# Kernel tuning notes

Measured on AMD Instinct MI355X. Metric: run time of the kernel, lower is better.

Reference implementation:

```python
import jax, jax.numpy as jnp
import numpy as np

EMBED_DIM = 1024
NUM_HEADS = 16
HEAD_DIM = EMBED_DIM // NUM_HEADS
ROPE_BASE = 10000.0


def _rope_cos_sin(seq_len, dim, dtype=jnp.float32):
    inv_freq = 1.0 / (ROPE_BASE ** (jnp.arange(0, dim, 2, dtype=jnp.float32) / dim))
    pos = jnp.arange(seq_len, dtype=jnp.float32)
    freqs = jnp.outer(pos, inv_freq)              # [S, dim/2]
    emb = jnp.concatenate([freqs, freqs], axis=-1)  # [S, dim]
    return jnp.cos(emb).astype(dtype), jnp.sin(emb).astype(dtype)


def _rotate_half(x):
    half = x.shape[-1] // 2
    return jnp.concatenate([-x[..., half:], x[..., :half]], axis=-1)


def setup_inputs() -> dict:
    key = jax.random.key(0)
    ks = jax.random.split(key, 12)
    B, S, E = 4, 2048, EMBED_DIM
    std = 1.0 / np.sqrt(E)
    inp = {
        'query': jax.random.normal(ks[0], (B, S, E), jnp.float32),
        'key': jax.random.normal(ks[1], (B, S, E), jnp.float32),
        'value': jax.random.normal(ks[2], (B, S, E), jnp.float32),
        'Wq': jax.random.uniform(ks[3], (E, E), jnp.float32, -std, std),
        'bq': jax.random.uniform(ks[4], (E,), jnp.float32, -std, std),
        'Wk': jax.random.uniform(ks[5], (E, E), jnp.float32, -std, std),
        'bk': jax.random.uniform(ks[6], (E,), jnp.float32, -std, std),
        'Wv': jax.random.uniform(ks[7], (E, E), jnp.float32, -std, std),
        'bv': jax.random.uniform(ks[8], (E,), jnp.float32, -std, std),
        'Wo': jax.random.uniform(ks[9], (E, E), jnp.float32, -std, std),
        'bo': jax.random.uniform(ks[10], (E,), jnp.float32, -std, std),
    }
    return inp


def reference(query, key, value, Wq, bq, Wk, bk, Wv, bv, Wo, bo):
    B, Sq, E = query.shape
    Sk = key.shape[1]
    H, D = NUM_HEADS, HEAD_DIM
    scale = D ** -0.5

    q = query @ Wq.T + bq
    k = key @ Wk.T + bk
    v = value @ Wv.T + bv

    # [B, H, S, D]
    q = q.reshape(B, Sq, H, D).transpose(0, 2, 1, 3)
    k = k.reshape(B, Sk, H, D).transpose(0, 2, 1, 3)
    v = v.reshape(B, Sk, H, D).transpose(0, 2, 1, 3)

    cos, sin = _rope_cos_sin(Sq, D, q.dtype)  # [S, D]; module slices by seq_len_q for both
    cos = cos[None, None]  # [1,1,S,D]
    sin = sin[None, None]
    q = q * cos + _rotate_half(q) * sin
    k = k * cos + _rotate_half(k) * sin

    scores = jnp.einsum('bhqd,bhkd->bhqk', q, k) * scale
    attn = jax.nn.softmax(scores, axis=-1)  # dropout p=0.0 -> identity
    out = jnp.einsum('bhqk,bhkd->bhqd', attn, v)
    out = out.transpose(0, 2, 1, 3).reshape(B, Sq, E)
    out = out @ Wo.T + bo
    attn_avg = attn.mean(axis=1)  # [B, Sq, Sk]
    return out, attn_avg
```

## Files before the change

### kernel.cpp

```cpp
#include <hip/hip_runtime.h>
#include <math.h>

#define TB 4
#define TS 2048
#define TE 1024
#define TH 16
#define TD 64
#define TM_ (TB*TS)

#define WS_Q   0
#define WS_K   8388608
#define WS_L   16777216
#define WS_TAB 16908288

typedef __attribute__((ext_vector_type(8))) short bf16x8;
typedef __attribute__((ext_vector_type(4))) float f32x4;

static __device__ inline unsigned fbits(float x) {
    union { float f; unsigned u; } v; v.f = x; return v.u;
}
static __device__ inline float bits2f(unsigned u) {
    union { unsigned u; float f; } v; v.u = u; return v.f;
}
static __device__ inline unsigned pack_rhu(float a, float b) {
    return __builtin_amdgcn_perm(fbits(b) + 0x8000u, fbits(a) + 0x8000u, 0x07060302u);
}
static __device__ inline short bf16s(float x) {
    return (short)((fbits(x) + 0x8000u) >> 16);
}
static __device__ inline void split2(float x0, float x1, unsigned& hp, unsigned& lp) {
    unsigned u0 = fbits(x0) + 0x8000u, u1 = fbits(x1) + 0x8000u;
    hp = __builtin_amdgcn_perm(u1, u0, 0x07060302u);
    float h0 = bits2f(u0 & 0xffff0000u);
    float h1 = bits2f(u1 & 0xffff0000u);
    lp = pack_rhu(x0 - h0, x1 - h1);
}

template<int MODE>
__global__ __launch_bounds__(256, 2)
void gemm_nt(const float* __restrict__ X, const float* __restrict__ W,
             const float* __restrict__ bias, float* __restrict__ out)
{
    __shared__ short Ah[128][40], Al[128][40];
    __shared__ short Bh[128][40], Bl[128][40];

    const int tid  = threadIdx.x;
    const int lane = tid & 63;
    const int wv   = tid >> 6;
    const int t16  = lane & 15;
    const int quad = lane >> 4;
    const int wm   = (wv >> 1) * 64;
    const int wn   = (wv & 1) * 64;
    const int m0 = blockIdx.y * 128;
    const int n0 = blockIdx.x * 128;
    const int K = TE, N = TE;

    const int srow = tid >> 1;
    const int skc  = (tid & 1) * 16;
    const float* Xp = X + (size_t)(m0 + srow) * K + skc;
    const float* Wp = W + (size_t)(n0 + srow) * K + skc;

    f32x4 acc[4][4];
    #pragma unroll
    for (int i = 0; i < 4; ++i)
        #pragma unroll
        for (int j = 0; j < 4; ++j) acc[i][j] = (f32x4){0.f, 0.f, 0.f, 0.f};

    for (int kt = 0; kt < K; kt += 32) {
        __syncthreads();
        {
            const float* xp = Xp + kt;
            float4 x0 = *(const float4*)(xp);
            float4 x1 = *(const float4*)(xp + 4);
            float4 x2 = *(const float4*)(xp + 8);
            float4 x3 = *(const float4*)(xp + 12);
            const float* wp = Wp + kt;
            float4 w0 = *(const float4*)(wp);
            float4 w1 = *(const float4*)(wp + 4);
            float4 w2 = *(const float4*)(wp + 8);
            float4 w3 = *(const float4*)(wp + 12);

            unsigned H[8], L[8];
            split2(x0.x, x0.y, H[0], L[0]);
            split2(x0.z, x0.w, H[1], L[1]);
            split2(x1.x, x1.y, H[2], L[2]);
            split2(x1.z, x1.w, H[3], L[3]);
            split2(x2.x, x2.y, H[4], L[4]);
            split2(x2.z, x2.w, H[5], L[5]);
            split2(x3.x, x3.y, H[6], L[6]);
            split2(x3.z, x3.w, H[7], L[7]);
            *(uint4*)&Ah[srow][skc]     = make_uint4(H[0], H[1], H[2], H[3]);
            *(uint4*)&Ah[srow][skc + 8] = make_uint4(H[4], H[5], H[6], H[7]);
            *(uint4*)&Al[srow][skc]     = make_uint4(L[0], L[1], L[2], L[3]);
            *(uint4*)&Al[srow][skc + 8] = make_uint4(L[4], L[5], L[6], L[7]);

            split2(w0.x, w0.y, H[0], L[0]);
            split2(w0.z, w0.w, H[1], L[1]);
            split2(w1.x, w1.y, H[2], L[2]);
            split2(w1.z, w1.w, H[3], L[3]);
            split2(w2.x, w2.y, H[4], L[4]);
            split2(w2.z, w2.w, H[5], L[5]);
            split2(w3.x, w3.y, H[6], L[6]);
            split2(w3.z, w3.w, H[7], L[7]);
            *(uint4*)&Bh[srow][skc]     = make_uint4(H[0], H[1], H[2], H[3]);
            *(uint4*)&Bh[srow][skc + 8] = make_uint4(H[4], H[5], H[6], H[7]);
            *(uint4*)&Bl[srow][skc]     = make_uint4(L[0], L[1], L[2], L[3]);
            *(uint4*)&Bl[srow][skc + 8] = make_uint4(L[4], L[5], L[6], L[7]);
        }
        __syncthreads();

        bf16x8 ah[4], al[4], bh[4], bl[4];
        #pragma unroll
        for (int i = 0; i < 4; ++i) {
            ah[i] = *(const bf16x8*)&Ah[wm + i * 16 + t16][quad * 8];
            al[i] = *(const bf16x8*)&Al[wm + i * 16 + t16][quad * 8];
            bh[i] = *(const bf16x8*)&Bh[wn + i * 16 + t16][quad * 8];
            bl[i] = *(const bf16x8*)&Bl[wn + i * 16 + t16][quad * 8];
        }
        #pragma unroll
        for (int i = 0; i < 4; ++i)
            #pragma unroll
            for (int j = 0; j < 4; ++j) {
                acc[i][j] = __builtin_amdgcn_mfma_f32_16x16x32_bf16(ah[i], bh[j], acc[i][j], 0, 0, 0);
                acc[i][j] = __builtin_amdgcn_mfma_f32_16x16x32_bf16(al[i], bh[j], acc[i][j], 0, 0, 0);
                acc[i][j] = __builtin_amdgcn_mfma_f32_16x16x32_bf16(ah[i], bl[j], acc[i][j], 0, 0, 0);
            }
    }

    if (MODE == 2) {
        short* o16 = (short*)out;
        const int b = m0 >> 11;
        const int sbase0 = (m0 & 2047) + wm + quad * 4;
        #pragma unroll
        for (int j = 0; j < 4; ++j) {
            const int n = n0 + wn + j * 16 + t16;
            const int h = n >> 6, d = n & 63;
            const float bv = bias[n];
            const size_t base = ((size_t)(b * TH + h) * TD + d) * TS;
            #pragma unroll
            for (int i = 0; i < 4; ++i) {
                const int s = sbase0 + i * 16;
                uint2 p = make_uint2(pack_rhu(acc[i][j][0] + bv, acc[i][j][1] + bv),
                                     pack_rhu(acc[i][j][2] + bv, acc[i][j][3] + bv));
                *(uint2*)(o16 + base + s) = p;
            }
        }
        return;
    }

    #pragma unroll
    for (int j = 0; j < 4; ++j) {
        const int n = n0 + wn + j * 16 + t16;
        const float bv = bias[n];
        if (MODE == 0) {
            #pragma unroll
            for (int i = 0; i < 4; ++i)
                #pragma unroll
                for (int r = 0; r < 4; ++r) {
                    const int m = m0 + wm + i * 16 + quad * 4 + r;
                    out[(size_t)m * N + n] = acc[i][j][r] + bv;
                }
        } else {
            const int h = n >> 6, d = n & 63;
            #pragma unroll
            for (int i = 0; i < 4; ++i)
                #pragma unroll
                for (int r = 0; r < 4; ++r) {
                    const int m = m0 + wm + i * 16 + quad * 4 + r;
                    const int bb_ = m >> 11, s = m & 2047;
                    out[((size_t)(bb_ * TH + h) * TS + s) * TD + d] = acc[i][j][r] + bv;
                }
        }
    }
}

__global__ void rope_table(float* __restrict__ tab)
{
    const int idx = blockIdx.x * 256 + threadIdx.x;
    const int d = idx & 31, s = idx >> 5;
    const float e = (float)(2 * d) / 64.0f;
    const float inv = 1.0f / powf(10000.0f, e);
    const float a = (float)s * inv;
    tab[2 * idx + 0] = cosf(a);
    tab[2 * idx + 1] = sinf(a);
}

__global__ void rope_apply(float* __restrict__ Q, float* __restrict__ Kv,
                           const float* __restrict__ tab)
{
    const int idx = blockIdx.x * 256 + threadIdx.x;
    const int half = TB * TH * TS * 32;
    float* P = (idx < half) ? Q : Kv;
    const int u = idx & (half - 1);
    const int d = u & 31;
    const int s = (u >> 5) & 2047;
    const int bh = u >> 16;
    const size_t base = (size_t)bh * (TS * TD) + (size_t)s * TD;
    const float c  = tab[2 * (s * 32 + d) + 0];
    const float sn = tab[2 * (s * 32 + d) + 1];
    const float x0 = P[base + d], x1 = P[base + d + 32];
    P[base + d]      = x0 * c - x1 * sn;
    P[base + d + 32] = x1 * c + x0 * sn;
}

__global__ __launch_bounds__(512, 4)
void attn_flash(const float* __restrict__ Q, const float* __restrict__ Kg,
                const short* __restrict__ VT, float* __restrict__ O,
                float* __restrict__ Ls)
{
    __shared__ short KhL[4096], KlL[4096];
    __shared__ short VtL[4096];
    __shared__ short PsL[8192];

    const int tid  = threadIdx.x;
    const int lane = tid & 63;
    const int wv   = tid >> 6;
    const int t16  = lane & 15;
    const int quad = lane >> 4;
    const int q0w  = wv * 16;

    const int L   = blockIdx.x + 16 * blockIdx.y + 256 * blockIdx.z;
    const int xcd = L & 7;
    const int i_  = L >> 3;
    const int qt  = i_ & 15;
    const int g   = (xcd << 3) | (i_ >> 4);
    const int h   = g & 15;
    const int b   = g >> 4;

    const int q0 = qt * 128;
    const int bh = b * TH + h;
    const size_t hoff = (size_t)bh * TS * TD;
    const float* Kr = Kg + hoff;
    const short* Vth = VT + (size_t)bh * TD * TS;

    const int cx0 = ((quad) ^ (t16 & 7)) * 8;
    const int cx1 = ((4 + quad) ^ (t16 & 7)) * 8;

    const float qsc = 0.125f * 1.44269504f;
    bf16x8 qfh[2], qfl[2];
    {
        const float* qp = Q + hoff + (size_t)(q0 + q0w + t16) * TD;
        #pragma unroll
        for (int ks = 0; ks < 2; ++ks) {
            float4 a = *(const float4*)(qp + ks * 32 + quad * 8);
            float4 c = *(const float4*)(qp + ks * 32 + quad * 8 + 4);
            union { unsigned u[4]; bf16x8 v; } H, Lo;
            split2(a.x * qsc, a.y * qsc, H.u[0], Lo.u[0]);
            split2(a.z * qsc, a.w * qsc, H.u[1], Lo.u[1]);
            split2(c.x * qsc, c.y * qsc, H.u[2], Lo.u[2]);
            split2(c.z * qsc, c.w * qsc, H.u[3], Lo.u[3]);
            qfh[ks] = H.v; qfl[ks] = Lo.v;
        }
    }

    float lsum[4] = {0.f, 0.f, 0.f, 0.f};
    f32x4 o_acc[4];
    #pragma unroll
    for (int dt = 0; dt < 4; ++dt) o_acc[dt] = (f32x4){0.f, 0.f, 0.f, 0.f};

    const int krow = tid >> 3;
    const int kch  = tid & 7;
    const int ksl  = (kch ^ (krow & 7)) * 8;

    for (int j0 = 0; j0 < TS; j0 += 64) {
        __syncthreads();
        {
            const float* kp = Kr + (size_t)(j0 + krow) * TD + kch * 8;
            float4 a = *(const float4*)kp;
            float4 c = *(const float4*)(kp + 4);
            unsigned H[4], Lo[4];
            split2(a.x, a.y, H[0], Lo[0]);
            split2(a.z, a.w, H[1], Lo[1]);
            split2(c.x, c.y, H[2], Lo[2]);
            split2(c.z, c.w, H[3], Lo[3]);
            *(uint4*)&KhL[krow * 64 + ksl] = make_uint4(H[0], H[1], H[2], H[3]);
            *(uint4*)&KlL[krow * 64 + ksl] = make_uint4(Lo[0], Lo[1], Lo[2], Lo[3]);
            uint4 vv = *(const uint4*)(Vth + (size_t)krow * TS + j0 + kch * 8);
            *(uint4*)&VtL[krow * 64 + ksl] = vv;
        }
        __syncthreads();

        f32x4 sc[4];
        #pragma unroll
        for (int t = 0; t < 4; ++t) sc[t] = (f32x4){0.f, 0.f, 0.f, 0.f};
        #pragma unroll
        for (int t = 0; t < 4; ++t) {
            const int rb = (t * 16 + t16) * 64;
            bf16x8 kh0 = *(const bf16x8*)&KhL[rb + cx0];
            bf16x8 kl0 = *(const bf16x8*)&KlL[rb + cx0];
            sc[t] = __builtin_amdgcn_mfma_f32_16x16x32_bf16(qfh[0], kh0, sc[t], 0, 0, 0);
            sc[t] = __builtin_amdgcn_mfma_f32_16x16x32_bf16(qfh[0], kl0, sc[t], 0, 0, 0);
            sc[t] = __builtin_amdgcn_mfma_f32_16x16x32_bf16(qfl[0], kh0, sc[t], 0, 0, 0);
            bf16x8 kh1 = *(const bf16x8*)&KhL[rb + cx1];
            bf16x8 kl1 = *(const bf16x8*)&KlL[rb + cx1];
            sc[t] = __builtin_amdgcn_mfma_f32_16x16x32_bf16(qfh[1], kh1, sc[t], 0, 0, 0);
            sc[t] = __builtin_amdgcn_mfma_f32_16x16x32_bf16(qfh[1], kl1, sc[t], 0, 0, 0);
            sc[t] = __builtin_amdgcn_mfma_f32_16x16x32_bf16(qfl[1], kh1, sc[t], 0, 0, 0);
        }

        #pragma unroll
        for (int t = 0; t < 4; ++t) {
            float p0 = __builtin_amdgcn_exp2f(sc[t][0]);
            float p1 = __builtin_amdgcn_exp2f(sc[t][1]);
            float p2 = __builtin_amdgcn_exp2f(sc[t][2]);
            float p3 = __builtin_amdgcn_exp2f(sc[t][3]);
            lsum[0] += p0; lsum[1] += p1; lsum[2] += p2; lsum[3] += p3;
            const int cb = 2 * t + (t16 >> 3);
            const int co = t16 & 7;
            const int r0 = q0w + quad * 4;
            PsL[(r0 + 0) * 64 + ((cb ^ ((r0 + 0) & 7)) * 8) + co] = bf16s(p0);
            PsL[(r0 + 1) * 64 + ((cb ^ ((r0 + 1) & 7)) * 8) + co] = bf16s(p1);
            PsL[(r0 + 2) * 64 + ((cb ^ ((r0 + 2) & 7)) * 8) + co] = bf16s(p2);
            PsL[(r0 + 3) * 64 + ((cb ^ ((r0 + 3) & 7)) * 8) + co] = bf16s(p3);
        }

        {
            const int pr = (q0w + t16) * 64;
            bf16x8 pa0 = *(const bf16x8*)&PsL[pr + cx0];
            #pragma unroll
            for (int dt = 0; dt < 4; ++dt) {
                bf16x8 vb = *(const bf16x8*)&VtL[(dt * 16 + t16) * 64 + cx0];
                o_acc[dt] = __builtin_amdgcn_mfma_f32_16x16x32_bf16(pa0, vb, o_acc[dt], 0, 0, 0);
            }
            bf16x8 pa1 = *(const bf16x8*)&PsL[pr + cx1];
            #pragma unroll
            for (int dt = 0; dt < 4; ++dt) {
                bf16x8 vb = *(const bf16x8*)&VtL[(dt * 16 + t16) * 64 + cx1];
                o_acc[dt] = __builtin_amdgcn_mfma_f32_16x16x32_bf16(pa1, vb, o_acc[dt], 0, 0, 0);
            }
        }
    }

    #pragma unroll
    for (int r = 0; r < 4; ++r) {
        #pragma unroll
        for (int off = 1; off < 16; off <<= 1)
            lsum[r] += __shfl_xor(lsum[r], off, 16);
    }

    #pragma unroll
    for (int r = 0; r < 4; ++r) {
        const int row = q0 + q0w + quad * 4 + r;
        const float inv = 1.0f / lsum[r];
        #pragma unroll
        for (int dt = 0; dt < 4; ++dt)
            O[((size_t)(b * TS) + row) * TE + h * TD + dt * 16 + t16] = o_acc[dt][r] * inv;
        if (t16 == 0)
            Ls[(size_t)bh * TS + row] = lsum[r];
    }
}

__global__ __launch_bounds__(256, 2)
void attn_avg_k(const float* __restrict__ Q, const float* __restrict__ Kg,
                const float* __restrict__ Ls, float* __restrict__ AV)
{
    __shared__ short Qt[128][72];
    __shared__ short Kt[128][72];
    __shared__ float ML[TH][128];

    const int tid  = threadIdx.x;
    const int lane = tid & 63;
    const int wv   = tid >> 6;
    const int t16  = lane & 15;
    const int quad = lane >> 4;
    const int wq = (wv >> 1) * 64;
    const int wj = (wv & 1) * 64;

    const int j0 = blockIdx.x * 128;
    const int q0 = blockIdx.y * 128;
    const int b  = blockIdx.z;

    #pragma unroll
    for (int i = 0; i < 8; ++i) {
        const int u = tid + 256 * i;
        const int h = u >> 7, r = u & 127;
        ML[h][r] = 1.0f / Ls[(size_t)(b * TH + h) * TS + q0 + r];
    }

    f32x4 acc[4][4];
    #pragma unroll
    for (int mt = 0; mt < 4; ++mt)
        #pragma unroll
        for (int nt = 0; nt < 4; ++nt) acc[mt][nt] = (f32x4){0.f, 0.f, 0.f, 0.f};

    const float qscale = 0.125f * 1.44269504f;

    for (int h = 0; h < TH; ++h) {
        __syncthreads();
        const size_t hoff = (size_t)(b * TH + h) * TS * TD;
        #pragma unroll
        for (int i = 0; i < 8; ++i) {
            const int f = tid + 256 * i;
            const int row = f >> 4;
            const int dq = (f & 15) * 4;
            float4 qv = *(const float4*)(Q + hoff + (size_t)(q0 + row) * TD + dq);
            uint2 qp = make_uint2(pack_rhu(qv.x * qscale, qv.y * qscale),
                                  pack_rhu(qv.z * qscale, qv.w * qscale));
            *(uint2*)&Qt[row][dq] = qp;
            float4 kv = *(const float4*)(Kg + hoff + (size_t)(j0 + row) * TD + dq);
            uint2 kp = make_uint2(pack_rhu(kv.x, kv.y), pack_rhu(kv.z, kv.w));
            *(uint2*)&Kt[row][dq] = kp;
        }
        __syncthreads();

        f32x4 sc[4][4];
        #pragma unroll
        for (int mt = 0; mt < 4; ++mt)
            #pragma unroll
            for (int nt = 0; nt < 4; ++nt) sc[mt][nt] = (f32x4){0.f, 0.f, 0.f, 0.f};
        #pragma unroll
        for (int ks = 0; ks < 2; ++ks) {
            bf16x8 af[4], bf[4];
            #pragma unroll
            for (int mt = 0; mt < 4; ++mt)
                af[mt] = *(const bf16x8*)&Qt[wq + mt * 16 + t16][ks * 32 + quad * 8];
            #pragma unroll
            for (int nt = 0; nt < 4; ++nt)
                bf[nt] = *(const bf16x8*)&Kt[wj + nt * 16 + t16][ks * 32 + quad * 8];
            #pragma unroll
            for (int mt = 0; mt < 4; ++mt)
                #pragma unroll
                for (int nt = 0; nt < 4; ++nt)
                    sc[mt][nt] = __builtin_amdgcn_mfma_f32_16x16x32_bf16(af[mt], bf[nt], sc[mt][nt], 0, 0, 0);
        }

        #pragma unroll
        for (int mt = 0; mt < 4; ++mt) {
            const int rl = wq + mt * 16 + quad * 4;
            const float lv[4] = {ML[h][rl], ML[h][rl + 1], ML[h][rl + 2], ML[h][rl + 3]};
            #pragma unroll
            for (int nt = 0; nt < 4; ++nt)
                #pragma unroll
                for (int r = 0; r < 4; ++r)
                    acc[mt][nt][r] = fmaf(__builtin_amdgcn_exp2f(sc[mt][nt][r]), lv[r], acc[mt][nt][r]);
        }
    }

    const float inv_h = 1.0f / (float)TH;
    #pragma unroll
    for (int mt = 0; mt < 4; ++mt) {
        #pragma unroll
        for (int r = 0; r < 4; ++r) {
            const int row = q0 + wq + mt * 16 + quad * 4 + r;
            #pragma unroll
            for (int nt = 0; nt < 4; ++nt) {
                const int col = j0 + wj + nt * 16 + t16;
                AV[((size_t)b * TS + row) * TS + col] = acc[mt][nt][r] * inv_h;
            }
        }
    }
}

extern "C" void kernel_launch(void* const* d_in, const int* in_sizes, int n_in,
                              void* d_out, int out_size, void* d_ws, size_t ws_size,
                              hipStream_t stream)
{
    const float* query = (const float*)d_in[0];
    const float* key   = (const float*)d_in[1];
    const float* value = (const float*)d_in[2];
    const float* Wq = (const float*)d_in[3];
    const float* bq = (const float*)d_in[4];
    const float* Wk = (const float*)d_in[5];
    const float* bk = (const float*)d_in[6];
    const float* Wv = (const float*)d_in[7];
    const float* bv = (const float*)d_in[8];
    const float* Wo = (const float*)d_in[9];
    const float* bo = (const float*)d_in[10];

    float* ws  = (float*)d_ws;
    float* Qr  = ws + WS_Q;
    float* Kr  = ws + WS_K;
    float* Lsf = ws + WS_L;
    float* tab = ws + WS_TAB;

    float* out  = (float*)d_out;
    float* attn = out + (size_t)TB * TS * TE;
    short* VT = (short*)attn;
    float* Ow = attn + 4194304;

    dim3 blk(256);
    dim3 gproj(TE / 128, TM_ / 128);

    gemm_nt<1><<<gproj, blk, 0, stream>>>(query, Wq, bq, Qr);
    gemm_nt<1><<<gproj, blk, 0, stream>>>(key,   Wk, bk, Kr);
    gemm_nt<2><<<gproj, blk, 0, stream>>>(value, Wv, bv, (float*)VT);
    rope_table<<<dim3(256), blk, 0, stream>>>(tab);
    rope_apply<<<dim3(32768), blk, 0, stream>>>(Qr, Kr, tab);
    attn_flash<<<dim3(TS / 128, TH, TB), dim3(512), 0, stream>>>(Qr, Kr, VT, Ow, Lsf);
    gemm_nt<0><<<gproj, blk, 0, stream>>>(Ow, Wo, bo, out);
    attn_avg_k<<<dim3(TS / 128, TS / 128, TB), blk, 0, stream>>>(Qr, Kr, Lsf, attn);
}
```

Baseline: 677.3 us.

## Pre-split weights and RoPE outputs into bf16 hi/lo once, prefetch K/V tiles

Adds a kernel that converts all four weight matrices into packed bf16 hi/lo pairs once, so the projection GEMMs load ready-made bf16 B tiles instead of re-splitting fp32 weights in every block. RoPE now also applies the softmax scale to Q, splits Q/K into swizzled bf16 hi/lo rows in place, and the attention and attn-average kernels read these directly. The flash kernel additionally register-prefetches the next K/V tile. This removes repeated conversion work and halves the global bytes read for K/Q, at the cost of an extra pass and scratch space carved from the output buffer.

Measured after the change: 685.7 us. Within noise of the previous version (+1.2%).

```diff
diff --git a/kernel.cpp b/kernel.cpp
--- a/kernel.cpp
+++ b/kernel.cpp
@@ -36,9 +36,35 @@
     lp = pack_rhu(x0 - h0, x1 - h1);
 }
 
+__global__ __launch_bounds__(256, 4)
+void wsplit(const float* __restrict__ W0, const float* __restrict__ W1,
+            const float* __restrict__ W2, const float* __restrict__ W3,
+            short* __restrict__ dst)
+{
+    const int idx = blockIdx.x * 256 + threadIdx.x;
+    const int t = idx & 31;
+    const int n = (idx >> 5) & 1023;
+    const int w = idx >> 15;
+    const float* W = (w == 0) ? W0 : (w == 1) ? W1 : (w == 2) ? W2 : W3;
+    const float* sp = W + (size_t)n * 1024 + t * 32;
+    short* dp = dst + ((size_t)(w * 1024 + n)) * 2048 + t * 64;
+    #pragma unroll
+    for (int c = 0; c < 4; ++c) {
+        float4 a = *(const float4*)(sp + c * 8);
+        float4 b = *(const float4*)(sp + c * 8 + 4);
+        unsigned H[4], L[4];
+        split2(a.x, a.y, H[0], L[0]);
+        split2(a.z, a.w, H[1], L[1]);
+        split2(b.x, b.y, H[2], L[2]);
+        split2(b.z, b.w, H[3], L[3]);
+        *(uint4*)(dp + c * 8)      = make_uint4(H[0], H[1], H[2], H[3]);
+        *(uint4*)(dp + 32 + c * 8) = make_uint4(L[0], L[1], L[2], L[3]);
+    }
+}
+
 template<int MODE>
 __global__ __launch_bounds__(256, 2)
-void gemm_nt(const float* __restrict__ X, const float* __restrict__ W,
+void gemm_nt(const float* __restrict__ X, const short* __restrict__ Wsp,
              const float* __restrict__ bias, float* __restrict__ out)
 {
     __shared__ short Ah[128][40], Al[128][40];
@@ -58,7 +84,7 @@
     const int srow = tid >> 1;
     const int skc  = (tid & 1) * 16;
     const float* Xp = X + (size_t)(m0 + srow) * K + skc;
-    const float* Wp = W + (size_t)(n0 + srow) * K + skc;
+    const short* Wp = Wsp + (size_t)(n0 + srow) * 2048 + skc;
 
     f32x4 acc[4][4];
     #pragma unroll
@@ -74,11 +100,11 @@
             float4 x1 = *(const float4*)(xp + 4);
             float4 x2 = *(const float4*)(xp + 8);
             float4 x3 = *(const float4*)(xp + 12);
-            const float* wp = Wp + kt;
-            float4 w0 = *(const float4*)(wp);
-            float4 w1 = *(const float4*)(wp + 4);
-            float4 w2 = *(const float4*)(wp + 8);
-            float4 w3 = *(const float4*)(wp + 12);
+            const short* wp = Wp + kt * 2;
+            uint4 wh0 = *(const uint4*)(wp);
+            uint4 wh1 = *(const uint4*)(wp + 8);
+            uint4 wl0 = *(const uint4*)(wp + 32);
+            uint4 wl1 = *(const uint4*)(wp + 40);
 
             unsigned H[8], L[8];
             split2(x0.x, x0.y, H[0], L[0]);
@@ -94,18 +120,10 @@
             *(uint4*)&Al[srow][skc]     = make_uint4(L[0], L[1], L[2], L[3]);
             *(uint4*)&Al[srow][skc + 8] = make_uint4(L[4], L[5], L[6], L[7]);
 
-            split2(w0.x, w0.y, H[0], L[0]);
-            split2(w0.z, w0.w, H[1], L[1]);
-            split2(w1.x, w1.y, H[2], L[2]);
-            split2(w1.z, w1.w, H[3], L[3]);
-            split2(w2.x, w2.y, H[4], L[4]);
-            split2(w2.z, w2.w, H[5], L[5]);
-            split2(w3.x, w3.y, H[6], L[6]);
-            split2(w3.z, w3.w, H[7], L[7]);
-            *(uint4*)&Bh[srow][skc]     = make_uint4(H[0], H[1], H[2], H[3]);
-            *(uint4*)&Bh[srow][skc + 8] = make_uint4(H[4], H[5], H[6], H[7]);
-            *(uint4*)&Bl[srow][skc]     = make_uint4(L[0], L[1], L[2], L[3]);
-            *(uint4*)&Bl[srow][skc + 8] = make_uint4(L[4], L[5], L[6], L[7]);
+            *(uint4*)&Bh[srow][skc]     = wh0;
+            *(uint4*)&Bh[srow][skc + 8] = wh1;
+            *(uint4*)&Bl[srow][skc]     = wl0;
+            *(uint4*)&Bl[srow][skc + 8] = wl1;
         }
         __syncthreads();
 
@@ -185,26 +203,48 @@
     tab[2 * idx + 1] = sinf(a);
 }
 
-__global__ void rope_apply(float* __restrict__ Q, float* __restrict__ Kv,
-                           const float* __restrict__ tab)
+__global__ __launch_bounds__(256, 2)
+void rope_split(float* __restrict__ Q, float* __restrict__ Kv,
+                const float* __restrict__ tab)
 {
     const int idx = blockIdx.x * 256 + threadIdx.x;
-    const int half = TB * TH * TS * 32;
-    float* P = (idx < half) ? Q : Kv;
-    const int u = idx & (half - 1);
-    const int d = u & 31;
-    const int s = (u >> 5) & 2047;
-    const int bh = u >> 16;
-    const size_t base = (size_t)bh * (TS * TD) + (size_t)s * TD;
-    const float c  = tab[2 * (s * 32 + d) + 0];
-    const float sn = tab[2 * (s * 32 + d) + 1];
-    const float x0 = P[base + d], x1 = P[base + d + 32];
-    P[base + d]      = x0 * c - x1 * sn;
-    P[base + d + 32] = x1 * c + x0 * sn;
+    const int s  = idx & 2047;
+    const int bh = (idx >> 11) & 63;
+    const int qk = idx >> 17;
+    float* P = qk ? Kv : Q;
+    const float scale = qk ? 1.0f : (0.125f * 1.44269504f);
+    const int key = qk ? (s & 7) : 0;
+    unsigned* rp = (unsigned*)(P + ((size_t)bh * TS + s) * 64);
+
+    unsigned xu[64];
+    #pragma unroll
+    for (int i = 0; i < 16; ++i) {
+        uint4 v = *(const uint4*)(rp + i * 4);
+        xu[4 * i + 0] = v.x; xu[4 * i + 1] = v.y;
+        xu[4 * i + 2] = v.z; xu[4 * i + 3] = v.w;
+    }
+    const float* tb = tab + (size_t)s * 64;
+    #pragma unroll
+    for (int d = 0; d < 32; ++d) {
+        const float c = tb[2 * d], sn = tb[2 * d + 1];
+        const float x0 = bits2f(xu[d]), x1 = bits2f(xu[d + 32]);
+        xu[d]      = fbits((x0 * c - x1 * sn) * scale);
+        xu[d + 32] = fbits((x1 * c + x0 * sn) * scale);
+    }
+    #pragma unroll
+    for (int ch = 0; ch < 8; ++ch) {
+        unsigned h[4], l[4];
+        #pragma unroll
+        for (int p = 0; p < 4; ++p)
+            split2(bits2f(xu[ch * 8 + 2 * p]), bits2f(xu[ch * 8 + 2 * p + 1]), h[p], l[p]);
+        const int slot = ch ^ key;
+        *(uint4*)(rp + slot * 4)      = make_uint4(h[0], h[1], h[2], h[3]);
+        *(uint4*)(rp + 32 + slot * 4) = make_uint4(l[0], l[1], l[2], l[3]);
+    }
 }
 
 __global__ __launch_bounds__(512, 4)
-void attn_flash(const float* __restrict__ Q, const float* __restrict__ Kg,
+void attn_flash(const short* __restrict__ Qs, const short* __restrict__ Ks,
                 const short* __restrict__ VT, float* __restrict__ O,
                 float* __restrict__ Ls)
 {
@@ -229,28 +269,19 @@
 
     const int q0 = qt * 128;
     const int bh = b * TH + h;
-    const size_t hoff = (size_t)bh * TS * TD;
-    const float* Kr = Kg + hoff;
+    const short* Krb = Ks + (size_t)bh * TS * 128;
     const short* Vth = VT + (size_t)bh * TD * TS;
 
     const int cx0 = ((quad) ^ (t16 & 7)) * 8;
     const int cx1 = ((4 + quad) ^ (t16 & 7)) * 8;
 
-    const float qsc = 0.125f * 1.44269504f;
     bf16x8 qfh[2], qfl[2];
     {
-        const float* qp = Q + hoff + (size_t)(q0 + q0w + t16) * TD;
-        #pragma unroll
-        for (int ks = 0; ks < 2; ++ks) {
-            float4 a = *(const float4*)(qp + ks * 32 + quad * 8);
-            float4 c = *(const float4*)(qp + ks * 32 + quad * 8 + 4);
-            union { unsigned u[4]; bf16x8 v; } H, Lo;
-            split2(a.x * qsc, a.y * qsc, H.u[0], Lo.u[0]);
-            split2(a.z * qsc, a.w * qsc, H.u[1], Lo.u[1]);
-            split2(c.x * qsc, c.y * qsc, H.u[2], Lo.u[2]);
-            split2(c.z * qsc, c.w * qsc, H.u[3], Lo.u[3]);
-            qfh[ks] = H.v; qfl[ks] = Lo.v;
-        }
+        const short* qrow = Qs + ((size_t)bh * TS + q0 + q0w + t16) * 128;
+        qfh[0] = *(const bf16x8*)(qrow + quad * 8);
+        qfh[1] = *(const bf16x8*)(qrow + 32 + quad * 8);
+        qfl[0] = *(const bf16x8*)(qrow + 64 + quad * 8);
+        qfl[1] = *(const bf16x8*)(qrow + 96 + quad * 8);
     }
 
     float lsum[4] = {0.f, 0.f, 0.f, 0.f};
@@ -262,23 +293,23 @@
     const int kch  = tid & 7;
     const int ksl  = (kch ^ (krow & 7)) * 8;
 
+    uint4 rkh = *(const uint4*)(Krb + (size_t)krow * 128 + kch * 8);
+    uint4 rkl = *(const uint4*)(Krb + (size_t)krow * 128 + 64 + kch * 8);
+    uint4 rvv = *(const uint4*)(Vth + (size_t)krow * TS + kch * 8);
+
     for (int j0 = 0; j0 < TS; j0 += 64) {
         __syncthreads();
-        {
-            const float* kp = Kr + (size_t)(j0 + krow) * TD + kch * 8;
-            float4 a = *(const float4*)kp;
-            float4 c = *(const float4*)(kp + 4);
-            unsigned H[4], Lo[4];
-            split2(a.x, a.y, H[0], Lo[0]);
-            split2(a.z, a.w, H[1], Lo[1]);
-            split2(c.x, c.y, H[2], Lo[2]);
-            split2(c.z, c.w, H[3], Lo[3]);
-            *(uint4*)&KhL[krow * 64 + ksl] = make_uint4(H[0], H[1], H[2], H[3]);
-            *(uint4*)&KlL[krow * 64 + ksl] = make_uint4(Lo[0], Lo[1], Lo[2], Lo[3]);
-            uint4 vv = *(const uint4*)(Vth + (size_t)krow * TS + j0 + kch * 8);
-            *(uint4*)&VtL[krow * 64 + ksl] = vv;
-        }
+        *(uint4*)&KhL[krow * 64 + kch * 8] = rkh;
+        *(uint4*)&KlL[krow * 64 + kch * 8] = rkl;
+        *(uint4*)&VtL[krow * 64 + ksl]     = rvv;
         __syncthreads();
+
+        if (j0 + 64 < TS) {
+            const short* kr = Krb + (size_t)(j0 + 64 + krow) * 128;
+            rkh = *(const uint4*)(kr + kch * 8);
+            rkl = *(const uint4*)(kr + 64 + kch * 8);
+            rvv = *(const uint4*)(Vth + (size_t)krow * TS + j0 + 64 + kch * 8);
+        }
 
         f32x4 sc[4];
         #pragma unroll
@@ -351,7 +382,7 @@
 }
 
 __global__ __launch_bounds__(256, 2)
-void attn_avg_k(const float* __restrict__ Q, const float* __restrict__ Kg,
+void attn_avg_k(const short* __restrict__ Qs, const short* __restrict__ Ks,
                 const float* __restrict__ Ls, float* __restrict__ AV)
 {
     __shared__ short Qt[128][72];
@@ -383,23 +414,18 @@
         #pragma unroll
         for (int nt = 0; nt < 4; ++nt) acc[mt][nt] = (f32x4){0.f, 0.f, 0.f, 0.f};
 
-    const float qscale = 0.125f * 1.44269504f;
-
     for (int h = 0; h < TH; ++h) {
         __syncthreads();
-        const size_t hoff = (size_t)(b * TH + h) * TS * TD;
-        #pragma unroll
-        for (int i = 0; i < 8; ++i) {
+        const size_t rbq = (size_t)(b * TH + h) * TS + q0;
+        const size_t rbk = (size_t)(b * TH + h) * TS + j0;
+        #pragma unroll
+        for (int i = 0; i < 4; ++i) {
             const int f = tid + 256 * i;
-            const int row = f >> 4;
-            const int dq = (f & 15) * 4;
-            float4 qv = *(const float4*)(Q + hoff + (size_t)(q0 + row) * TD + dq);
-            uint2 qp = make_uint2(pack_rhu(qv.x * qscale, qv.y * qscale),
-                                  pack_rhu(qv.z * qscale, qv.w * qscale));
-            *(uint2*)&Qt[row][dq] = qp;
-            float4 kv = *(const float4*)(Kg + hoff + (size_t)(j0 + row) * TD + dq);
-            uint2 kp = make_uint2(pack_rhu(kv.x, kv.y), pack_rhu(kv.z, kv.w));
-            *(uint2*)&Kt[row][dq] = kp;
+            const int row = f >> 3, c = f & 7;
+            *(uint4*)&Qt[row][c * 8] =
+                *(const uint4*)(Qs + (rbq + row) * 128 + c * 8);
+            *(uint4*)&Kt[row][(c ^ (row & 7)) * 8] =
+                *(const uint4*)(Ks + (rbk + row) * 128 + c * 8);
         }
         __syncthreads();
 
@@ -475,18 +501,27 @@
 
     float* out  = (float*)d_out;
     float* attn = out + (size_t)TB * TS * TE;
-    short* VT = (short*)attn;
-    float* Ow = attn + 4194304;
+    short* VT   = (short*)attn;
+    float* Ow   = attn + 4194304;
+    short* Wsp4 = (short*)(attn + 12582912);
 
     dim3 blk(256);
     dim3 gproj(TE / 128, TM_ / 128);
 
-    gemm_nt<1><<<gproj, blk, 0, stream>>>(query, Wq, bq, Qr);
-    gemm_nt<1><<<gproj, blk, 0, stream>>>(key,   Wk, bk, Kr);
-    gemm_nt<2><<<gproj, blk, 0, stream>>>(value, Wv, bv, (float*)VT);
+    wsplit<<<dim3(512), blk, 0, stream>>>(Wq, Wk, Wv, Wo, Wsp4);
     rope_table<<<dim3(256), blk, 0, stream>>>(tab);
-    rope_apply<<<dim3(32768), blk, 0, stream>>>(Qr, Kr, tab);
-    attn_flash<<<dim3(TS / 128, TH, TB), dim3(512), 0, stream>>>(Qr, Kr, VT, Ow, Lsf);
-    gemm_nt<0><<<gproj, blk, 0, stream>>>(Ow, Wo, bo, out);
-    attn_avg_k<<<dim3(TS / 128, TS / 128, TB), blk, 0, stream>>>(Qr, Kr, Lsf, attn);
-}
+
+    gemm_nt<1><<<gproj, blk, 0, stream>>>(query, Wsp4,               bq, Qr);
+    gemm_nt<1><<<gproj, blk, 0, stream>>>(key,   Wsp4 + 2097152,     bk, Kr);
+    gemm_nt<2><<<gproj, blk, 0, stream>>>(value, Wsp4 + 2 * 2097152, bv, (float*)VT);
+
+    rope_split<<<dim3(1024), blk, 0, stream>>>(Qr, Kr, tab);
+
+    attn_flash<<<dim3(TS / 128, TH, TB), dim3(512), 0, stream>>>(
+        (const short*)Qr, (const short*)Kr, VT, Ow, Lsf);
+
+    gemm_nt<0><<<gproj, blk, 0, stream>>>(Ow, Wsp4 + 3 * 2097152, bo, out);
+
+    attn_avg_k<<<dim3(TS / 128, TS / 128, TB), blk, 0, stream>>>(
+        (const short*)Qr, (const short*)Kr, Lsf, attn);
+}
```
